# Performance work log

Hardware: AMD Instinct MI355X
Metric: run time of the kernel (lower is better)

Reference implementation:

```python
import jax, jax.numpy as jnp
import numpy as np

NUM_NODES = 100000
NUM_HYPEREDGES = 20000
NUM_SEMALINKS = 5000
NUM_EDGES = 600000
IN_DIM = 128
SIGNAL_DIM = 64
OUT_DIM = 128


def setup_inputs() -> dict:
    key = jax.random.key(0)
    k = jax.random.split(key, 8)
    node_embeddings = jax.random.normal(k[0], (NUM_NODES, IN_DIM), dtype=jnp.float32)
    semalink_embeddings = jax.random.normal(k[1], (NUM_SEMALINKS, SIGNAL_DIM), dtype=jnp.float32)
    hyperedge_embeddings = jax.random.normal(k[2], (NUM_HYPEREDGES, IN_DIM), dtype=jnp.float32)
    node_idx = jax.random.randint(k[3], (NUM_EDGES,), 0, NUM_NODES, dtype=jnp.int32)
    sl_idx = jax.random.randint(k[4], (NUM_EDGES,), 0, NUM_SEMALINKS, dtype=jnp.int32)
    he_idx = jax.random.randint(k[5], (NUM_EDGES,), 0, NUM_HYPEREDGES, dtype=jnp.int32)
    semalinks = jnp.stack([node_idx, sl_idx, he_idx], axis=1)  # [E, 3]
    W_a = jax.random.normal(k[6], (IN_DIM, SIGNAL_DIM), dtype=jnp.float32)
    W_f = jax.random.normal(k[7], (2 * IN_DIM, OUT_DIM), dtype=jnp.float32)
    return {
        'node_embeddings': node_embeddings,
        'semalink_embeddings': semalink_embeddings,
        'hyperedge_embeddings': hyperedge_embeddings,
        'semalinks': semalinks,
        'W_a': W_a,
        'W_f': W_f,
    }


def reference(node_embeddings, semalink_embeddings, hyperedge_embeddings, semalinks, W_a, W_f):
    # Original loops edges in order, ASSIGNING final_embeddings[node_idx] each time:
    # only the LAST edge touching each node determines that node's output.
    E = semalinks.shape[0]
    n_idx = semalinks[:, 0]
    s_idx = semalinks[:, 1]
    h_idx = semalinks[:, 2]

    order = jnp.arange(E, dtype=jnp.int32)
    last = jax.ops.segment_max(order, n_idx, num_segments=NUM_NODES)  # [N]
    has_edge = last >= 0
    last_c = jnp.clip(last, 0, E - 1)

    sel_h = h_idx[last_c]  # [N]
    sel_s = s_idx[last_c]  # [N]
    h_emb = hyperedge_embeddings[sel_h]          # [N, in_dim]
    sl_emb = semalink_embeddings[sel_s]          # [N, signal_dim]

    # per-node attention score (1x1 in original)
    r_h = node_embeddings @ W_a                  # [N, signal_dim]
    r_t = h_emb @ W_a                            # [N, signal_dim]
    score = jnp.sum(r_h * jnp.tanh(r_t + sl_emb), axis=-1, keepdims=True)  # [N, 1]
    gamma = jax.nn.softmax(score, axis=-1)       # softmax over singleton == 1.0 (same as torch)
    f = gamma * h_emb                            # [N, in_dim]

    u = jnp.concatenate([f, node_embeddings], axis=-1) @ W_f  # [N, out_dim]
    out = jnp.where(has_edge[:, None], u, jnp.zeros((), dtype=u.dtype))
    return out
```

## Files before the change

kernel.cpp:

```cpp
#include <hip/hip_runtime.h>
#include <hip/hip_bf16.h>

#define NNODES 100000
#define NHE 20000
#define NEDGES 600000

typedef float f32x4 __attribute__((ext_vector_type(4)));
typedef short bf16x8 __attribute__((ext_vector_type(8)));
typedef short bf16x4 __attribute__((ext_vector_type(4)));

__device__ __forceinline__ unsigned short f2bf(float f) {
    unsigned u = __builtin_bit_cast(unsigned, f);
    u += 0x7fffu + ((u >> 16) & 1u);
    return (unsigned short)(u >> 16);
}

__global__ void k_init(int* last) {
    int i = blockIdx.x * 256 + threadIdx.x;
    if (i < NNODES) last[i] = -1;
}

__global__ void k_scatter(const int* __restrict__ sl, int* __restrict__ last) {
    int e = blockIdx.x * 256 + threadIdx.x;
    if (e < NEDGES) atomicMax(&last[sl[3 * e]], e);
}

__global__ void k_prep_w(const float* __restrict__ Wf, unsigned short* __restrict__ wt) {
    int idx = blockIdx.x * 256 + threadIdx.x;
    int k = idx >> 7, c = idx & 127;
    float v = Wf[idx];
    int chunk = k >> 6, kk = k & 63;
    int byte = (c * 128 + kk * 2) ^ ((c & 7) << 4);
    wt[chunk * 8192 + (byte >> 1)] = f2bf(v);
}

__global__ __launch_bounds__(256) void k_main(
    const float* __restrict__ node_emb,
    const float* __restrict__ he_emb,
    const int* __restrict__ sl,
    const int* __restrict__ last,
    const unsigned short* __restrict__ wt,
    float* __restrict__ out)
{
    __shared__ __align__(16) unsigned short Xs[128 * 64];
    __shared__ __align__(16) unsigned short Ws[64 * 128];
    __shared__ int he_s[128];
    __shared__ int valid_s[128];

    int t = threadIdx.x;
    int r0 = blockIdx.x * 128;

    if (t < 128) {
        int ri = r0 + t;
        int e = (ri < NNODES) ? last[ri] : -1;
        int v = (e >= 0) ? 1 : 0;
        he_s[t] = v ? sl[3 * e + 2] : 0;
        valid_s[t] = v;
    }
    __syncthreads();

    int lane = t & 63, w = t >> 6;
    int wm = w >> 1, wn = w & 1;
    int l15 = lane & 15, l4 = lane >> 4;

    f32x4 acc[4][4] = {};

    for (int kc = 0; kc < 4; ++kc) {
        #pragma unroll
        for (int i = 0; i < 8; ++i) {
            int idx = i * 256 + t;
            int row = idx >> 4;
            int q = idx & 15;
            const float* src;
            if (kc < 2) {
                int hr = he_s[row];
                src = he_emb + hr * 128 + kc * 64 + q * 4;
            } else {
                int ri = r0 + row;
                if (ri >= NNODES) ri = NNODES - 1;
                src = node_emb + ri * 128 + (kc - 2) * 64 + q * 4;
            }
            f32x4 v = *(const f32x4*)src;
            bf16x4 p;
            p[0] = (short)f2bf(v[0]);
            p[1] = (short)f2bf(v[1]);
            p[2] = (short)f2bf(v[2]);
            p[3] = (short)f2bf(v[3]);
            int byte = (row * 128 + q * 8) ^ ((row & 7) << 4);
            *(bf16x4*)((char*)Xs + byte) = p;
        }
        {
            const f32x4* src = (const f32x4*)(wt + kc * 8192);
            f32x4* dst = (f32x4*)Ws;
            #pragma unroll
            for (int i = 0; i < 4; ++i) {
                int idx = i * 256 + t;
                dst[idx] = src[idx];
            }
        }
        __syncthreads();

        #pragma unroll
        for (int ks = 0; ks < 2; ++ks) {
            bf16x8 af[4], bw[4];
            #pragma unroll
            for (int fm = 0; fm < 4; ++fm) {
                int row = wm * 64 + fm * 16 + l15;
                int byte = (row * 128 + ks * 64 + l4 * 16) ^ ((row & 7) << 4);
                af[fm] = *(const bf16x8*)((const char*)Xs + byte);
            }
            #pragma unroll
            for (int fn = 0; fn < 4; ++fn) {
                int rc = wn * 64 + fn * 16 + l15;
                int byte = (rc * 128 + ks * 64 + l4 * 16) ^ ((rc & 7) << 4);
                bw[fn] = *(const bf16x8*)((const char*)Ws + byte);
            }
            #pragma unroll
            for (int fm = 0; fm < 4; ++fm)
                #pragma unroll
                for (int fn = 0; fn < 4; ++fn)
                    acc[fm][fn] = __builtin_amdgcn_mfma_f32_16x16x32_bf16(
                        af[fm], bw[fn], acc[fm][fn], 0, 0, 0);
        }
        __syncthreads();
    }

    #pragma unroll
    for (int fm = 0; fm < 4; ++fm) {
        #pragma unroll
        for (int j = 0; j < 4; ++j) {
            int lrow = wm * 64 + fm * 16 + l4 * 4 + j;
            int ri = r0 + lrow;
            if (ri < NNODES) {
                int v = valid_s[lrow];
                #pragma unroll
                for (int fn = 0; fn < 4; ++fn) {
                    int col = wn * 64 + fn * 16 + l15;
                    out[ri * 128 + col] = v ? acc[fm][fn][j] : 0.0f;
                }
            }
        }
    }
}

extern "C" void kernel_launch(void* const* d_in, const int* in_sizes, int n_in,
                              void* d_out, int out_size, void* d_ws, size_t ws_size,
                              hipStream_t stream) {
    const float* node_emb = (const float*)d_in[0];
    const float* he_emb = (const float*)d_in[2];
    const int* sl = (const int*)d_in[3];
    const float* Wf = (const float*)d_in[5];
    float* out = (float*)d_out;

    int* last = (int*)d_ws;
    unsigned short* wt = (unsigned short*)((char*)d_ws + 400128);

    k_init<<<(NNODES + 255) / 256, 256, 0, stream>>>(last);
    k_scatter<<<(NEDGES + 255) / 256, 256, 0, stream>>>(sl, last);
    k_prep_w<<<128, 256, 0, stream>>>(Wf, wt);
    k_main<<<(NNODES + 127) / 128, 256, 0, stream>>>(node_emb, he_emb, sl, last, wt, out);
}
```

Measured before the change: 78.35 us.

## Double-buffer activation tiles, read weights from global, shrink tiles, merge setup kernels

Merges the init and weight-prep kernels into one launch and stores the weights as plain column-major bf16 that is read straight from global/L2 instead of being staged in shared memory. The main kernel now uses 64-row tiles, giving twice as many blocks, and double-buffers the activation tile in LDS. Next-chunk global loads are held in registers while the current chunk computes, and one barrier per step replaces two. The risk is more global weight traffic per block and a hand-rolled barrier that relies on the double buffer to avoid write-after-read races.

Measured after the change: 78.37 us. No clear change (+0.0%).

```diff
diff --git a/kernel.cpp b/kernel.cpp
--- a/kernel.cpp
+++ b/kernel.cpp
@@ -15,23 +15,22 @@
     return (unsigned short)(u >> 16);
 }
 
-__global__ void k_init(int* last) {
-    int i = blockIdx.x * 256 + threadIdx.x;
-    if (i < NNODES) last[i] = -1;
+__global__ void k_setup(int* __restrict__ last, const float* __restrict__ Wf,
+                        unsigned short* __restrict__ wt) {
+    int b = blockIdx.x, t = threadIdx.x;
+    if (b < 391) {
+        int i = b * 256 + t;
+        if (i < NNODES) last[i] = -1;
+    } else {
+        int idx = (b - 391) * 256 + t;
+        int k = idx >> 7, c = idx & 127;
+        wt[c * 256 + k] = f2bf(Wf[idx]);
+    }
 }
 
 __global__ void k_scatter(const int* __restrict__ sl, int* __restrict__ last) {
     int e = blockIdx.x * 256 + threadIdx.x;
     if (e < NEDGES) atomicMax(&last[sl[3 * e]], e);
-}
-
-__global__ void k_prep_w(const float* __restrict__ Wf, unsigned short* __restrict__ wt) {
-    int idx = blockIdx.x * 256 + threadIdx.x;
-    int k = idx >> 7, c = idx & 127;
-    float v = Wf[idx];
-    int chunk = k >> 6, kk = k & 63;
-    int byte = (c * 128 + kk * 2) ^ ((c & 7) << 4);
-    wt[chunk * 8192 + (byte >> 1)] = f2bf(v);
 }
 
 __global__ __launch_bounds__(256) void k_main(
@@ -42,94 +41,98 @@
     const unsigned short* __restrict__ wt,
     float* __restrict__ out)
 {
-    __shared__ __align__(16) unsigned short Xs[128 * 64];
-    __shared__ __align__(16) unsigned short Ws[64 * 128];
-    __shared__ int he_s[128];
-    __shared__ int valid_s[128];
+    __shared__ __align__(16) unsigned short Xs[2][64 * 64];
+    __shared__ int he_s[64];
+    __shared__ int valid_s[64];
 
     int t = threadIdx.x;
-    int r0 = blockIdx.x * 128;
+    int r0 = blockIdx.x * 64;
 
-    if (t < 128) {
+    if (t < 64) {
         int ri = r0 + t;
         int e = (ri < NNODES) ? last[ri] : -1;
         int v = (e >= 0) ? 1 : 0;
+        valid_s[t] = v;
         he_s[t] = v ? sl[3 * e + 2] : 0;
-        valid_s[t] = v;
     }
     __syncthreads();
 
     int lane = t & 63, w = t >> 6;
     int wm = w >> 1, wn = w & 1;
     int l15 = lane & 15, l4 = lane >> 4;
+    int tr = t >> 4, q = t & 15;
 
-    f32x4 acc[4][4] = {};
+    f32x4 acc[2][4] = {};
+    f32x4 pre[4];
 
+    #pragma unroll
+    for (int i = 0; i < 4; ++i) {
+        int row = i * 16 + tr;
+        pre[i] = *(const f32x4*)(he_emb + he_s[row] * 128 + q * 4);
+    }
+
+    #pragma unroll
     for (int kc = 0; kc < 4; ++kc) {
         #pragma unroll
-        for (int i = 0; i < 8; ++i) {
-            int idx = i * 256 + t;
-            int row = idx >> 4;
-            int q = idx & 15;
-            const float* src;
-            if (kc < 2) {
-                int hr = he_s[row];
-                src = he_emb + hr * 128 + kc * 64 + q * 4;
-            } else {
-                int ri = r0 + row;
-                if (ri >= NNODES) ri = NNODES - 1;
-                src = node_emb + ri * 128 + (kc - 2) * 64 + q * 4;
-            }
-            f32x4 v = *(const f32x4*)src;
+        for (int i = 0; i < 4; ++i) {
+            int row = i * 16 + tr;
             bf16x4 p;
-            p[0] = (short)f2bf(v[0]);
-            p[1] = (short)f2bf(v[1]);
-            p[2] = (short)f2bf(v[2]);
-            p[3] = (short)f2bf(v[3]);
+            p[0] = (short)f2bf(pre[i][0]);
+            p[1] = (short)f2bf(pre[i][1]);
+            p[2] = (short)f2bf(pre[i][2]);
+            p[3] = (short)f2bf(pre[i][3]);
             int byte = (row * 128 + q * 8) ^ ((row & 7) << 4);
-            *(bf16x4*)((char*)Xs + byte) = p;
+            *(bf16x4*)((char*)Xs[kc & 1] + byte) = p;
         }
-        {
-            const f32x4* src = (const f32x4*)(wt + kc * 8192);
-            f32x4* dst = (f32x4*)Ws;
+        if (kc < 3) {
+            int kn = kc + 1;
             #pragma unroll
             for (int i = 0; i < 4; ++i) {
-                int idx = i * 256 + t;
-                dst[idx] = src[idx];
+                int row = i * 16 + tr;
+                const float* s;
+                if (kn < 2) {
+                    s = he_emb + he_s[row] * 128 + kn * 64 + q * 4;
+                } else {
+                    int ri = r0 + row;
+                    if (ri >= NNODES) ri = NNODES - 1;
+                    s = node_emb + ri * 128 + (kn - 2) * 64 + q * 4;
+                }
+                pre[i] = *(const f32x4*)s;
             }
         }
-        __syncthreads();
+        asm volatile("s_waitcnt lgkmcnt(0)" ::: "memory");
+        __builtin_amdgcn_sched_barrier(0);
+        __builtin_amdgcn_s_barrier();
+        __builtin_amdgcn_sched_barrier(0);
 
         #pragma unroll
         for (int ks = 0; ks < 2; ++ks) {
-            bf16x8 af[4], bw[4];
+            bf16x8 a[2], b[4];
             #pragma unroll
-            for (int fm = 0; fm < 4; ++fm) {
-                int row = wm * 64 + fm * 16 + l15;
+            for (int fm = 0; fm < 2; ++fm) {
+                int row = wm * 32 + fm * 16 + l15;
                 int byte = (row * 128 + ks * 64 + l4 * 16) ^ ((row & 7) << 4);
-                af[fm] = *(const bf16x8*)((const char*)Xs + byte);
+                a[fm] = *(const bf16x8*)((const char*)Xs[kc & 1] + byte);
             }
             #pragma unroll
             for (int fn = 0; fn < 4; ++fn) {
-                int rc = wn * 64 + fn * 16 + l15;
-                int byte = (rc * 128 + ks * 64 + l4 * 16) ^ ((rc & 7) << 4);
-                bw[fn] = *(const bf16x8*)((const char*)Ws + byte);
+                int col = wn * 64 + fn * 16 + l15;
+                b[fn] = *(const bf16x8*)(wt + col * 256 + kc * 64 + ks * 32 + l4 * 8);
             }
             #pragma unroll
-            for (int fm = 0; fm < 4; ++fm)
+            for (int fm = 0; fm < 2; ++fm)
                 #pragma unroll
                 for (int fn = 0; fn < 4; ++fn)
                     acc[fm][fn] = __builtin_amdgcn_mfma_f32_16x16x32_bf16(
-                        af[fm], bw[fn], acc[fm][fn], 0, 0, 0);
+                        a[fm], b[fn], acc[fm][fn], 0, 0, 0);
         }
-        __syncthreads();
     }
 
     #pragma unroll
-    for (int fm = 0; fm < 4; ++fm) {
+    for (int fm = 0; fm < 2; ++fm) {
         #pragma unroll
         for (int j = 0; j < 4; ++j) {
-            int lrow = wm * 64 + fm * 16 + l4 * 4 + j;
+            int lrow = wm * 32 + fm * 16 + l4 * 4 + j;
             int ri = r0 + lrow;
             if (ri < NNODES) {
                 int v = valid_s[lrow];
@@ -155,8 +158,7 @@
     int* last = (int*)d_ws;
     unsigned short* wt = (unsigned short*)((char*)d_ws + 400128);
 
-    k_init<<<(NNODES + 255) / 256, 256, 0, stream>>>(last);
+    k_setup<<<519, 256, 0, stream>>>(last, Wf, wt);
     k_scatter<<<(NEDGES + 255) / 256, 256, 0, stream>>>(sl, last);
-    k_prep_w<<<128, 256, 0, stream>>>(Wf, wt);
-    k_main<<<(NNODES + 127) / 128, 256, 0, stream>>>(node_emb, he_emb, sl, last, wt, out);
+    k_main<<<(NNODES + 63) / 64, 256, 0, stream>>>(node_emb, he_emb, sl, last, wt, out);
 }
```
